# Kernel optimization log

Measured on AMD Instinct MI355X. Metric: run time of the kernel, lower is better.

## Reference

```python
import jax, jax.numpy as jnp
import numpy as np

TAU = [1, 2, 4, 8]
B, T, FC, FX = 128, 2048, 512, 512


def setup_inputs() -> dict:
    key = jax.random.key(0)
    k1, k2, k3, k4 = jax.random.split(key, 4)
    C = jax.random.normal(k1, (B, T, FC), dtype=jnp.float32)
    X = jax.random.normal(k2, (B, T, FX), dtype=jnp.float32)
    # one Linear(encoding_size -> context_size) per tau; torch weight layout [out, in]
    W = jax.random.normal(k3, (len(TAU), FC, FX), dtype=jnp.float32) * (1.0 / np.sqrt(FX))
    b = jax.random.normal(k4, (len(TAU), FC), dtype=jnp.float32) * 0.01
    return {"C": C, "X": X, "W": W, "b": b}


def _infonce(Ct, Xe, Wk, bk):
    # Ct: [B, Tt, fc], Xe: [B, Tt, fx]
    Xt = jnp.einsum('btf,gf->btg', Xe, Wk) + bk          # Linear: [B, Tt, fc]
    Z = jnp.einsum('itf,jtf->ijt', Ct, Xt)               # scores [B, B, Tt]
    Zmax = jnp.max(Z, axis=1, keepdims=True)             # [B, 1, Tt]
    lse = jnp.log(jnp.sum(jnp.exp(Z - Zmax), axis=1)) + Zmax[:, 0]  # [B, Tt]
    Zdiag = jnp.diagonal(Z, axis1=0, axis2=1).T          # Z[i,i,t] -> [B, Tt]
    return jnp.mean(Zdiag - lse)


def reference(C, X, W, b):
    losses = [_infonce(C[:, :-t], X[:, t:], W[k], b[k]) for k, t in enumerate(TAU)]
    return jnp.stack(losses)
```

## Files before the change

### kernel.cpp

```cpp
#include <hip/hip_runtime.h>
#include <math.h>

constexpr int Tn  = 2048;
constexpr int FCn = 512;
constexpr int FXn = 512;
constexpr int SXW = 72;
constexpr int SYC = 136;
constexpr int SZS = 132;

typedef __attribute__((ext_vector_type(8))) short  bf16x8;
typedef __attribute__((ext_vector_type(4))) float  f32x4;

__device__ __forceinline__ unsigned pk2(float a, float b) {
  return __builtin_amdgcn_perm(__float_as_uint(b), __float_as_uint(a), 0x07060302u);
}
__device__ __forceinline__ uint4 pack8(float4 a, float4 b) {
  uint4 rv;
  rv.x = pk2(a.x, a.y); rv.y = pk2(a.z, a.w);
  rv.z = pk2(b.x, b.y); rv.w = pk2(b.z, b.w);
  return rv;
}

__device__ __forceinline__ void gll16(const unsigned short* g, void* lds) {
  __builtin_amdgcn_global_load_lds(
      (const __attribute__((address_space(1))) unsigned int*)g,
      (__attribute__((address_space(3))) unsigned int*)lds, 16, 0, 0);
}

__global__ void zero4(float* out) {
  if (threadIdx.x < 4) out[threadIdx.x] = 0.0f;
}

__global__ void finalize4(float* out) {
  int k = threadIdx.x;
  if (k < 4) out[k] *= 1.0f / (128.0f * (float)(Tn - (1 << k)));
}

__global__ void tobf16(const float* __restrict__ s, unsigned short* __restrict__ d) {
  int i = blockIdx.x * 256 + threadIdx.x;
  float4 v = ((const float4*)s)[i];
  uint2 p; p.x = pk2(v.x, v.y); p.y = pk2(v.z, v.w);
  ((uint2*)d)[i] = p;
}

__global__ __launch_bounds__(256, 2)
void infonce_v7(const float* __restrict__ Cp, const unsigned short* __restrict__ Xb,
                const unsigned short* __restrict__ Wb, float* __restrict__ out)
{
  __shared__ __align__(16) unsigned char smem[67648];
  char* sm   = (char*)smem;
  char* sWc  = sm + 16384;
  float* sZ  = (float*)sm;
  float* sRed = (float*)(sm + 67584);

  const int tid  = threadIdx.x;
  const int lane = tid & 63;
  const int wave = tid >> 6;
  const int r    = lane & 15;
  const int h    = lane >> 4;
  const int jw   = wave >> 1;
  const int gw   = wave & 1;
  const int iw   = wave >> 1;
  const int jw2  = wave & 1;

  const int orig = blockIdx.x;
  const int xcd  = orig & 7;
  const int loc  = orig >> 3;
  const int wg   = (xcd < 4) ? (xcd * 1024 + loc) : (4096 + (xcd - 4) * 1023 + loc);
  const int k    = wg & 3;
  const int t    = wg >> 2;
  const int tau  = 1 << k;
  if (t >= Tn - tau) return;
  const int s = t + tau;

  const int colg = (lane & 7) ^ (lane >> 3);
  const unsigned short* xlane = Xb + (size_t)(wave * 32 + (lane >> 3)) * (Tn * FXn)
                                + (size_t)s * FXn + colg * 8;
  const unsigned short* wlane = Wb + (size_t)k * (FCn * FXn)
                                + (size_t)(wave * 64 + (lane >> 3)) * FXn + colg * 8;
  char* xdst = sm  + wave * 4096;
  char* wdst = sWc + wave * 8192;

  const float* cr0 = Cp + (size_t)(iw * 64 +  0 + r) * (Tn * FCn) + (size_t)t * FCn;
  const float* cr1 = Cp + (size_t)(iw * 64 + 16 + r) * (Tn * FCn) + (size_t)t * FCn;
  const float* cr2 = Cp + (size_t)(iw * 64 + 32 + r) * (Tn * FCn) + (size_t)t * FCn;
  const float* cr3 = Cp + (size_t)(iw * 64 + 48 + r) * (Tn * FCn) + (size_t)t * FCn;

  f32x4 zacc[4][4];
#pragma unroll
  for (int a = 0; a < 4; ++a)
#pragma unroll
    for (int b = 0; b < 4; ++b) zacc[a][b] = f32x4{0.f, 0.f, 0.f, 0.f};

#pragma unroll 1
  for (int gc = 0; gc < 2; ++gc) {
    f32x4 yacc[4][8];
#pragma unroll
    for (int a = 0; a < 4; ++a)
#pragma unroll
      for (int b = 0; b < 8; ++b) yacc[a][b] = f32x4{0.f, 0.f, 0.f, 0.f};

#pragma unroll 1
    for (int xc = 0; xc < 8; ++xc) {
      __syncthreads();
#pragma unroll
      for (int i = 0; i < 4; ++i)
        gll16(xlane + (size_t)(i * 8) * (Tn * FXn) + xc * 64, xdst + i * 1024);
#pragma unroll
      for (int i = 0; i < 8; ++i)
        gll16(wlane + (size_t)(gc * 256 + i * 8) * FXn + xc * 64, wdst + i * 1024);
      __syncthreads();
#pragma unroll
      for (int ks = 0; ks < 2; ++ks) {
        const int cbx = (ks * 64 + h * 16) ^ ((r & 7) << 4);
        bf16x8 ax[4], bw[8];
#pragma unroll
        for (int bm = 0; bm < 4; ++bm)
          ax[bm] = *(const bf16x8*)(sm + (jw * 64 + bm * 16 + r) * 128 + cbx);
#pragma unroll
        for (int bn = 0; bn < 8; ++bn)
          bw[bn] = *(const bf16x8*)(sWc + (gw * 128 + bn * 16 + r) * 128 + cbx);
#pragma unroll
        for (int bm = 0; bm < 4; ++bm)
#pragma unroll
          for (int bn = 0; bn < 8; ++bn)
            yacc[bm][bn] = __builtin_amdgcn_mfma_f32_16x16x32_bf16(
                ax[bm], bw[bn], yacc[bm][bn], 0, 0, 0);
      }
    }
    __syncthreads();
#pragma unroll
    for (int bm = 0; bm < 4; ++bm)
#pragma unroll
      for (int bn = 0; bn < 8; ++bn)
#pragma unroll
        for (int reg = 0; reg < 4; ++reg) {
          const int row = jw * 64 + bm * 16 + h * 4 + reg;
          const int col = gw * 128 + bn * 16 + r;
          *(unsigned short*)(sm + row * 528 + col * 2) =
              (unsigned short)(__float_as_uint(yacc[bm][bn][reg]) >> 16);
        }
    __syncthreads();
#pragma unroll 2
    for (int ks2 = 0; ks2 < 8; ++ks2) {
      const int goff = gc * 256 + ks2 * 32 + h * 8;
      const int gb   = ks2 * 64 + h * 16;
      bf16x8 ac[4], by[4];
      {
        float4 u0 = *(const float4*)(cr0 + goff);
        float4 v0 = *(const float4*)(cr0 + goff + 4);
        float4 u1 = *(const float4*)(cr1 + goff);
        float4 v1 = *(const float4*)(cr1 + goff + 4);
        float4 u2 = *(const float4*)(cr2 + goff);
        float4 v2 = *(const float4*)(cr2 + goff + 4);
        float4 u3 = *(const float4*)(cr3 + goff);
        float4 v3 = *(const float4*)(cr3 + goff + 4);
        ac[0] = __builtin_bit_cast(bf16x8, pack8(u0, v0));
        ac[1] = __builtin_bit_cast(bf16x8, pack8(u1, v1));
        ac[2] = __builtin_bit_cast(bf16x8, pack8(u2, v2));
        ac[3] = __builtin_bit_cast(bf16x8, pack8(u3, v3));
      }
#pragma unroll
      for (int bn = 0; bn < 4; ++bn)
        by[bn] = *(const bf16x8*)(sm + (jw2 * 64 + bn * 16 + r) * 528 + gb);
#pragma unroll
      for (int bm = 0; bm < 4; ++bm)
#pragma unroll
        for (int bn = 0; bn < 4; ++bn)
          zacc[bm][bn] = __builtin_amdgcn_mfma_f32_16x16x32_bf16(
              ac[bm], by[bn], zacc[bm][bn], 0, 0, 0);
    }
  }
  __syncthreads();
#pragma unroll
  for (int bm = 0; bm < 4; ++bm)
#pragma unroll
    for (int bn = 0; bn < 4; ++bn)
#pragma unroll
      for (int reg = 0; reg < 4; ++reg)
        sZ[(iw * 64 + bm * 16 + h * 4 + reg) * SZS + (jw2 * 64 + bn * 16 + r)] =
            zacc[bm][bn][reg];
  __syncthreads();

  const int row = wave * 32 + (lane >> 1);
  const int c0l = lane & 1;
  float mx = -3.4e38f;
#pragma unroll
  for (int m = 0; m < 64; ++m) mx = fmaxf(mx, sZ[row * SZS + c0l + m * 2]);
  mx = fmaxf(mx, __shfl_xor(mx, 1));
  float sum = 0.f;
#pragma unroll
  for (int m = 0; m < 64; ++m) sum += __expf(sZ[row * SZS + c0l + m * 2] - mx);
  sum += __shfl_xor(sum, 1);
  float val = (c0l == 0) ? (sZ[row * SZS + row] - (__logf(sum) + mx)) : 0.f;
#pragma unroll
  for (int off = 1; off < 64; off <<= 1) val += __shfl_xor(val, off);
  if (lane == 0) sRed[wave] = val;
  __syncthreads();
  if (tid == 0) atomicAdd(out + k, sRed[0] + sRed[1] + sRed[2] + sRed[3]);
}

template <bool WBF>
__global__ __launch_bounds__(512, 4)
void infonce_main(const float* __restrict__ Cp, const float* __restrict__ Xp,
                  const void* __restrict__ Wp, float* __restrict__ out)
{
  __shared__ __align__(16) unsigned char smem[71680];
  unsigned short* sX = (unsigned short*)(smem);
  unsigned short* sW = (unsigned short*)(smem + 18432);
  unsigned short* sY = (unsigned short*)(smem + 36864);
  unsigned short* sC = (unsigned short*)(smem);
  float* sZ   = (float*)(smem);
  float* sRed = (float*)(smem + 67584);

  const int tid  = threadIdx.x;
  const int lane = tid & 63;
  const int wave = tid >> 6;
  const int r    = lane & 15;
  const int h    = lane >> 4;
  const int wr   = wave >> 1;
  const int wc   = wave & 1;

  const int orig = blockIdx.x;
  const int xcd  = orig & 7;
  const int loc  = orig >> 3;
  const int wg   = (xcd < 4) ? (xcd * 1024 + loc) : (4096 + (xcd - 4) * 1023 + loc);
  const int k    = wg & 3;
  const int t    = wg >> 2;
  const int tau  = 1 << k;
  if (t >= Tn - tau) return;

  const float* Cb = Cp + (size_t)t * FCn;
  const float* Xb = Xp + (size_t)(t + tau) * FXn;

  const int srow = tid >> 2;
  const int scol = (tid & 3) * 16;
  const float* xs = Xb + (size_t)srow * (Tn * FXn) + scol;
  unsigned short* xd = sX + srow * SXW + scol;
  unsigned short* wd = sW + srow * SXW + scol;
  const unsigned short* wsh = (const unsigned short*)Wp + (size_t)k * (FCn * FXn)
                              + (size_t)srow * FXn + scol;
  const float* wsf = (const float*)Wp + (size_t)k * (FCn * FXn)
                     + (size_t)srow * FXn + scol;
  const int crow0 = tid >> 4;
  const int ccol  = (tid & 15) * 8;
  const float* cs = Cb + (size_t)crow0 * (Tn * FCn) + ccol;
  unsigned short* cd = sC + crow0 * SYC + ccol;
  const size_t cstep = (size_t)32 * Tn * FCn;

  float4 px0, px1, px2, px3;
  float4 pw0, pw1, pw2, pw3;
  uint4  pb0, pb1;
  float4 pc0, pc1, pc2, pc3, pc4, pc5, pc6, pc7;

#define LOAD_X(XC) do { \
    const float4* _p = (const float4*)(xs + (XC) * 64); \
    px0 = _p[0]; px1 = _p[1]; px2 = _p[2]; px3 = _p[3]; } while (0)
#define LOAD_W(GC, XC) do { \
    if constexpr (WBF) { \
      const uint4* _p = (const uint4*)(wsh + (size_t)((GC) * 128) * FXn + (XC) * 64); \
      pb0 = _p[0]; pb1 = _p[1]; \
    } else { \
      const float4* _p = (const float4*)(wsf + (size_t)((GC) * 128) * FXn + (XC) * 64); \
      pw0 = _p[0]; pw1 = _p[1]; pw2 = _p[2]; pw3 = _p[3]; } } while (0)
#define STORE_XW() do { \
    *(uint4*)(xd)     = pack8(px0, px1); \
    *(uint4*)(xd + 8) = pack8(px2, px3); \
    if constexpr (WBF) { *(uint4*)(wd) = pb0; *(uint4*)(wd + 8) = pb1; } \
    else { *(uint4*)(wd) = pack8(pw0, pw1); *(uint4*)(wd + 8) = pack8(pw2, pw3); } \
  } while (0)
#define MFMA_Y() do { \
    _Pragma("unroll") \
    for (int ks = 0; ks < 2; ++ks) { \
      const int xoo = ks * 32 + h * 8; \
      bf16x8 a0 = *(const bf16x8*)(sX + (wr * 32 + 0  + r) * SXW + xoo); \
      bf16x8 a1 = *(const bf16x8*)(sX + (wr * 32 + 16 + r) * SXW + xoo); \
      _Pragma("unroll") \
      for (int bg = 0; bg < 4; ++bg) { \
        bf16x8 bb = *(const bf16x8*)(sW + (wc * 64 + bg * 16 + r) * SXW + xoo); \
        yacc[0][bg] = __builtin_amdgcn_mfma_f32_16x16x32_bf16(a0, bb, yacc[0][bg], 0, 0, 0); \
        yacc[1][bg] = __builtin_amdgcn_mfma_f32_16x16x32_bf16(a1, bb, yacc[1][bg], 0, 0, 0); \
      } } } while (0)

  f32x4 zacc[2][4];
#pragma unroll
  for (int a = 0; a < 2; ++a)
#pragma unroll
    for (int b = 0; b < 4; ++b) zacc[a][b] = f32x4{0.f, 0.f, 0.f, 0.f};

  LOAD_X(0); LOAD_W(0, 0);

  for (int gc = 0; gc < 4; ++gc) {
    f32x4 yacc[2][4];
#pragma unroll
    for (int a = 0; a < 2; ++a)
#pragma unroll
      for (int b = 0; b < 4; ++b) yacc[a][b] = f32x4{0.f, 0.f, 0.f, 0.f};

    for (int xc = 0; xc < 7; ++xc) {
      __syncthreads();
      STORE_XW();
      __syncthreads();
      LOAD_X(xc + 1); LOAD_W(gc, xc + 1);
      MFMA_Y();
    }
    __syncthreads();
    STORE_XW();
    __syncthreads();
    {
      const float4* p0 = (const float4*)(cs + 0 * cstep + gc * 128);
      const float4* p1 = (const float4*)(cs + 1 * cstep + gc * 128);
      const float4* p2 = (const float4*)(cs + 2 * cstep + gc * 128);
      const float4* p3 = (const float4*)(cs + 3 * cstep + gc * 128);
      pc0 = p0[0]; pc1 = p0[1];
      pc2 = p1[0]; pc3 = p1[1];
      pc4 = p2[0]; pc5 = p2[1];
      pc6 = p3[0]; pc7 = p3[1];
    }
    MFMA_Y();

#pragma unroll
    for (int aj = 0; aj < 2; ++aj)
#pragma unroll
      for (int bg = 0; bg < 4; ++bg)
#pragma unroll
        for (int reg = 0; reg < 4; ++reg)
          sY[(wr * 32 + aj * 16 + h * 4 + reg) * SYC + (wc * 64 + bg * 16 + r)] =
              (unsigned short)(__float_as_uint(yacc[aj][bg][reg]) >> 16);
    __syncthreads();
    *(uint4*)(cd + 0 * 32 * SYC) = pack8(pc0, pc1);
    *(uint4*)(cd + 1 * 32 * SYC) = pack8(pc2, pc3);
    *(uint4*)(cd + 2 * 32 * SYC) = pack8(pc4, pc5);
    *(uint4*)(cd + 3 * 32 * SYC) = pack8(pc6, pc7);
    __syncthreads();
    if (gc < 3) { LOAD_X(0); LOAD_W(gc + 1, 0); }
#pragma unroll
    for (int ks = 0; ks < 4; ++ks) {
      const int go = ks * 32 + h * 8;
      bf16x8 a0 = *(const bf16x8*)(sC + (wr * 32 + 0  + r) * SYC + go);
      bf16x8 a1 = *(const bf16x8*)(sC + (wr * 32 + 16 + r) * SYC + go);
#pragma unroll
      for (int bj = 0; bj < 4; ++bj) {
        bf16x8 bb = *(const bf16x8*)(sY + (wc * 64 + bj * 16 + r) * SYC + go);
        zacc[0][bj] = __builtin_amdgcn_mfma_f32_16x16x32_bf16(a0, bb, zacc[0][bj], 0, 0, 0);
        zacc[1][bj] = __builtin_amdgcn_mfma_f32_16x16x32_bf16(a1, bb, zacc[1][bj], 0, 0, 0);
      }
    }
  }
  __syncthreads();
#pragma unroll
  for (int ai = 0; ai < 2; ++ai)
#pragma unroll
    for (int bj = 0; bj < 4; ++bj)
#pragma unroll
      for (int reg = 0; reg < 4; ++reg)
        sZ[(wr * 32 + ai * 16 + h * 4 + reg) * SZS + (wc * 64 + bj * 16 + r)] =
            zacc[ai][bj][reg];
  __syncthreads();

  const int row = wave * 16 + (lane >> 2);
  const int c0l = lane & 3;
  float mx = -3.4e38f;
#pragma unroll
  for (int m = 0; m < 32; ++m) mx = fmaxf(mx, sZ[row * SZS + c0l + m * 4]);
  mx = fmaxf(mx, __shfl_xor(mx, 1));
  mx = fmaxf(mx, __shfl_xor(mx, 2));
  float sum = 0.f;
#pragma unroll
  for (int m = 0; m < 32; ++m) sum += __expf(sZ[row * SZS + c0l + m * 4] - mx);
  sum += __shfl_xor(sum, 1);
  sum += __shfl_xor(sum, 2);
  float val = (c0l == 0) ? (sZ[row * SZS + row] - (__logf(sum) + mx)) : 0.f;
#pragma unroll
  for (int off = 1; off < 64; off <<= 1) val += __shfl_xor(val, off);
  if (lane == 0) sRed[wave] = val;
  __syncthreads();
  if (tid == 0) {
    float bs = 0.f;
#pragma unroll
    for (int w2 = 0; w2 < 8; ++w2) bs += sRed[w2];
    atomicAdd(out + k, bs);
  }
#undef LOAD_X
#undef LOAD_W
#undef STORE_XW
#undef MFMA_Y
}

extern "C" void kernel_launch(void* const* d_in, const int* in_sizes, int n_in,
                              void* d_out, int out_size, void* d_ws, size_t ws_size,
                              hipStream_t stream) {
  const float* C = (const float*)d_in[0];
  const float* X = (const float*)d_in[1];
  const float* W = (const float*)d_in[2];
  float* out = (float*)d_out;

  const size_t NX = (size_t)128 * Tn * FXn;
  const size_t NW = (size_t)4 * FCn * FXn;
  const size_t WS_W   = NW * 2;
  const size_t WS_MID = WS_W + NX * 2;

  hipLaunchKernelGGL(zero4, dim3(1), dim3(64), 0, stream, out);

  if (ws_size >= WS_MID) {
    unsigned short* Wbf = (unsigned short*)d_ws;
    unsigned short* Xbf = (unsigned short*)((char*)d_ws + WS_W);
    hipLaunchKernelGGL(tobf16, dim3((unsigned)(NW / 1024)), dim3(256), 0, stream, W, Wbf);
    hipLaunchKernelGGL(tobf16, dim3((unsigned)(NX / 1024)), dim3(256), 0, stream, X, Xbf);
    hipLaunchKernelGGL(infonce_v7, dim3(2047 * 4), dim3(256), 0, stream,
                       C, Xbf, Wbf, out);
  } else if (ws_size >= WS_W) {
    hipLaunchKernelGGL(tobf16, dim3((unsigned)(NW / 1024)), dim3(256), 0, stream,
                       W, (unsigned short*)d_ws);
    hipLaunchKernelGGL(infonce_main<true>, dim3(2047 * 4), dim3(512), 0, stream,
                       C, X, (const void*)d_ws, out);
  } else {
    hipLaunchKernelGGL(infonce_main<false>, dim3(2047 * 4), dim3(512), 0, stream,
                       C, X, (const void*)W, out);
  }
  hipLaunchKernelGGL(finalize4, dim3(1), dim3(64), 0, stream, out);
}
```

Measured before the change: 1.364 ms.

## Double-buffer X/W staging and compute softmax stats from MFMA registers

The projection GEMM now stages X and W in 32-element k-chunks into two LDS buffers. The next chunk's global_load_lds is issued before the current chunk's MFMAs, so load latency overlaps compute and each step needs one barrier instead of two. The Y tile is stored in LDS with an XOR swizzle instead of padded rows. The final logsumexp now reduces max and sum directly from the Z accumulator registers using lane shuffles and a small cross-wave stats exchange, which avoids the full Z round trip through LDS. The cost is more LDS buffer bookkeeping and extra shuffle and barrier steps in the epilogue.

```diff
diff --git a/kernel.cpp b/kernel.cpp
--- a/kernel.cpp
+++ b/kernel.cpp
@@ -44,24 +44,24 @@
 }
 
 __global__ __launch_bounds__(256, 2)
-void infonce_v7(const float* __restrict__ Cp, const unsigned short* __restrict__ Xb,
+void infonce_v8(const float* __restrict__ Cp, const unsigned short* __restrict__ Xb,
                 const unsigned short* __restrict__ Wb, float* __restrict__ out)
 {
   __shared__ __align__(16) unsigned char smem[67648];
-  char* sm   = (char*)smem;
-  char* sWc  = sm + 16384;
-  float* sZ  = (float*)sm;
-  float* sRed = (float*)(sm + 67584);
-
-  const int tid  = threadIdx.x;
-  const int lane = tid & 63;
-  const int wave = tid >> 6;
-  const int r    = lane & 15;
-  const int h    = lane >> 4;
-  const int jw   = wave >> 1;
-  const int gw   = wave & 1;
-  const int iw   = wave >> 1;
-  const int jw2  = wave & 1;
+  char* sm = (char*)smem;
+  float* stats_m = (float*)(sm + 65536);
+  float* stats_s = (float*)(sm + 66560);
+  float* sRed    = (float*)(sm + 67584);
+
+  const int tid = threadIdx.x;
+  const int l   = tid & 63;
+  const int w   = tid >> 6;
+  const int r   = l & 15;
+  const int h   = l >> 4;
+  const int jw  = w >> 1;
+  const int gw  = w & 1;
+  const int iw  = w >> 1;
+  const int jw2 = w & 1;
 
   const int orig = blockIdx.x;
   const int xcd  = orig & 7;
@@ -73,62 +73,83 @@
   if (t >= Tn - tau) return;
   const int s = t + tau;
 
-  const int colg = (lane & 7) ^ (lane >> 3);
-  const unsigned short* xlane = Xb + (size_t)(wave * 32 + (lane >> 3)) * (Tn * FXn)
-                                + (size_t)s * FXn + colg * 8;
-  const unsigned short* wlane = Wb + (size_t)k * (FCn * FXn)
-                                + (size_t)(wave * 64 + (lane >> 3)) * FXn + colg * 8;
-  char* xdst = sm  + wave * 4096;
-  char* wdst = sWc + wave * 8192;
-
-  const float* cr0 = Cp + (size_t)(iw * 64 +  0 + r) * (Tn * FCn) + (size_t)t * FCn;
-  const float* cr1 = Cp + (size_t)(iw * 64 + 16 + r) * (Tn * FCn) + (size_t)t * FCn;
-  const float* cr2 = Cp + (size_t)(iw * 64 + 32 + r) * (Tn * FCn) + (size_t)t * FCn;
-  const float* cr3 = Cp + (size_t)(iw * 64 + 48 + r) * (Tn * FCn) + (size_t)t * FCn;
+  const int sub = l >> 2;
+  const int gsw = (l & 3) ^ ((l >> 3) & 3);
+  const size_t xstr = (size_t)Tn * FXn;
+  const unsigned short* xs0 = Xb + (size_t)(w * 32 + sub) * xstr
+                              + (size_t)s * FXn + gsw * 8;
+  const unsigned short* xs1 = xs0 + (size_t)16 * xstr;
+  const unsigned short* wk  = Wb + (size_t)k * (FCn * FXn) + gsw * 8;
+  const unsigned short* ws0 = wk  + (size_t)(w * 64 + sub) * FXn;
+  const unsigned short* ws1 = ws0 + (size_t)16 * FXn;
+  const unsigned short* ws2 = ws0 + (size_t)32 * FXn;
+  const unsigned short* ws3 = ws0 + (size_t)48 * FXn;
+
+  const size_t cstr = (size_t)Tn * FCn;
+  const float* cr0 = Cp + (size_t)(iw * 64 +  0 + r) * cstr + (size_t)t * FCn;
+  const float* cr1 = Cp + (size_t)(iw * 64 + 16 + r) * cstr + (size_t)t * FCn;
+  const float* cr2 = Cp + (size_t)(iw * 64 + 32 + r) * cstr + (size_t)t * FCn;
+  const float* cr3 = Cp + (size_t)(iw * 64 + 48 + r) * cstr + (size_t)t * FCn;
 
   f32x4 zacc[4][4];
 #pragma unroll
   for (int a = 0; a < 4; ++a)
 #pragma unroll
     for (int b = 0; b < 4; ++b) zacc[a][b] = f32x4{0.f, 0.f, 0.f, 0.f};
+
+#define STG8(BUFC, XC) do { \
+    char* _bb = sm + (BUFC) * 24576; \
+    const size_t _xo = (size_t)(XC) * 32; \
+    gll16(xs0 + _xo, _bb + (w * 2    ) * 1024); \
+    gll16(xs1 + _xo, _bb + (w * 2 + 1) * 1024); \
+    const size_t _wo = wgc + _xo; \
+    gll16(ws0 + _wo, _bb + 8192 + (w * 4    ) * 1024); \
+    gll16(ws1 + _wo, _bb + 8192 + (w * 4 + 1) * 1024); \
+    gll16(ws2 + _wo, _bb + 8192 + (w * 4 + 2) * 1024); \
+    gll16(ws3 + _wo, _bb + 8192 + (w * 4 + 3) * 1024); \
+  } while (0)
+
+#define MFY8(BUFC) do { \
+    const char* _bx = sm + (BUFC) * 24576; \
+    const char* _bw = _bx + 8192; \
+    const int _gb = (h ^ ((r >> 1) & 3)) << 4; \
+    bf16x8 _ax[4]; \
+    _Pragma("unroll") \
+    for (int _bm = 0; _bm < 4; ++_bm) \
+      _ax[_bm] = *(const bf16x8*)(_bx + (jw * 64 + _bm * 16 + r) * 64 + _gb); \
+    bf16x8 _bv[8]; \
+    _Pragma("unroll") \
+    for (int _bn = 0; _bn < 8; ++_bn) \
+      _bv[_bn] = *(const bf16x8*)(_bw + (gw * 128 + _bn * 16 + r) * 64 + _gb); \
+    _Pragma("unroll") \
+    for (int _bm = 0; _bm < 4; ++_bm) \
+      _Pragma("unroll") \
+      for (int _bn = 0; _bn < 8; ++_bn) \
+        yacc[_bm][_bn] = __builtin_amdgcn_mfma_f32_16x16x32_bf16( \
+            _ax[_bm], _bv[_bn], yacc[_bm][_bn], 0, 0, 0); \
+  } while (0)
 
 #pragma unroll 1
   for (int gc = 0; gc < 2; ++gc) {
+    const size_t wgc = (size_t)gc * 256 * FXn;
     f32x4 yacc[4][8];
 #pragma unroll
     for (int a = 0; a < 4; ++a)
 #pragma unroll
       for (int b = 0; b < 8; ++b) yacc[a][b] = f32x4{0.f, 0.f, 0.f, 0.f};
 
+    STG8(0, 0);
+    __syncthreads();
 #pragma unroll 1
-    for (int xc = 0; xc < 8; ++xc) {
+    for (int xc2 = 0; xc2 < 8; ++xc2) {
+      STG8(1, 2 * xc2 + 1);
+      MFY8(0);
       __syncthreads();
-#pragma unroll
-      for (int i = 0; i < 4; ++i)
-        gll16(xlane + (size_t)(i * 8) * (Tn * FXn) + xc * 64, xdst + i * 1024);
-#pragma unroll
-      for (int i = 0; i < 8; ++i)
-        gll16(wlane + (size_t)(gc * 256 + i * 8) * FXn + xc * 64, wdst + i * 1024);
+      if (xc2 < 7) STG8(0, 2 * xc2 + 2);
+      MFY8(1);
       __syncthreads();
-#pragma unroll
-      for (int ks = 0; ks < 2; ++ks) {
-        const int cbx = (ks * 64 + h * 16) ^ ((r & 7) << 4);
-        bf16x8 ax[4], bw[8];
-#pragma unroll
-        for (int bm = 0; bm < 4; ++bm)
-          ax[bm] = *(const bf16x8*)(sm + (jw * 64 + bm * 16 + r) * 128 + cbx);
-#pragma unroll
-        for (int bn = 0; bn < 8; ++bn)
-          bw[bn] = *(const bf16x8*)(sWc + (gw * 128 + bn * 16 + r) * 128 + cbx);
-#pragma unroll
-        for (int bm = 0; bm < 4; ++bm)
-#pragma unroll
-          for (int bn = 0; bn < 8; ++bn)
-            yacc[bm][bn] = __builtin_amdgcn_mfma_f32_16x16x32_bf16(
-                ax[bm], bw[bn], yacc[bm][bn], 0, 0, 0);
-      }
-    }
-    __syncthreads();
+    }
+
 #pragma unroll
     for (int bm = 0; bm < 4; ++bm)
 #pragma unroll
@@ -137,67 +158,98 @@
         for (int reg = 0; reg < 4; ++reg) {
           const int row = jw * 64 + bm * 16 + h * 4 + reg;
           const int col = gw * 128 + bn * 16 + r;
-          *(unsigned short*)(sm + row * 528 + col * 2) =
+          *(unsigned short*)(sm + row * 512 + ((col * 2) ^ ((row & 7) << 4))) =
               (unsigned short)(__float_as_uint(yacc[bm][bn][reg]) >> 16);
         }
     __syncthreads();
+
+    const int swz = (r & 7) << 4;
 #pragma unroll 2
     for (int ks2 = 0; ks2 < 8; ++ks2) {
       const int goff = gc * 256 + ks2 * 32 + h * 8;
-      const int gb   = ks2 * 64 + h * 16;
-      bf16x8 ac[4], by[4];
-      {
-        float4 u0 = *(const float4*)(cr0 + goff);
-        float4 v0 = *(const float4*)(cr0 + goff + 4);
-        float4 u1 = *(const float4*)(cr1 + goff);
-        float4 v1 = *(const float4*)(cr1 + goff + 4);
-        float4 u2 = *(const float4*)(cr2 + goff);
-        float4 v2 = *(const float4*)(cr2 + goff + 4);
-        float4 u3 = *(const float4*)(cr3 + goff);
-        float4 v3 = *(const float4*)(cr3 + goff + 4);
-        ac[0] = __builtin_bit_cast(bf16x8, pack8(u0, v0));
-        ac[1] = __builtin_bit_cast(bf16x8, pack8(u1, v1));
-        ac[2] = __builtin_bit_cast(bf16x8, pack8(u2, v2));
-        ac[3] = __builtin_bit_cast(bf16x8, pack8(u3, v3));
-      }
+      float4 u0 = *(const float4*)(cr0 + goff), p0 = *(const float4*)(cr0 + goff + 4);
+      float4 u1 = *(const float4*)(cr1 + goff), p1 = *(const float4*)(cr1 + goff + 4);
+      float4 u2 = *(const float4*)(cr2 + goff), p2 = *(const float4*)(cr2 + goff + 4);
+      float4 u3 = *(const float4*)(cr3 + goff), p3 = *(const float4*)(cr3 + goff + 4);
+      bf16x8 acv[4];
+      acv[0] = __builtin_bit_cast(bf16x8, pack8(u0, p0));
+      acv[1] = __builtin_bit_cast(bf16x8, pack8(u1, p1));
+      acv[2] = __builtin_bit_cast(bf16x8, pack8(u2, p2));
+      acv[3] = __builtin_bit_cast(bf16x8, pack8(u3, p3));
+      const int gb = ks2 * 64 + h * 16;
+      bf16x8 byv[4];
 #pragma unroll
       for (int bn = 0; bn < 4; ++bn)
-        by[bn] = *(const bf16x8*)(sm + (jw2 * 64 + bn * 16 + r) * 528 + gb);
+        byv[bn] = *(const bf16x8*)(sm + (jw2 * 64 + bn * 16 + r) * 512 + (gb ^ swz));
 #pragma unroll
       for (int bm = 0; bm < 4; ++bm)
 #pragma unroll
         for (int bn = 0; bn < 4; ++bn)
           zacc[bm][bn] = __builtin_amdgcn_mfma_f32_16x16x32_bf16(
-              ac[bm], by[bn], zacc[bm][bn], 0, 0, 0);
-    }
+              acv[bm], byv[bn], zacc[bm][bn], 0, 0, 0);
+    }
+    __syncthreads();
   }
-  __syncthreads();
+
+  float gm[4][4], tot[4][4];
 #pragma unroll
   for (int bm = 0; bm < 4; ++bm)
 #pragma unroll
-    for (int bn = 0; bn < 4; ++bn)
+    for (int reg = 0; reg < 4; ++reg) {
+      float m = fmaxf(fmaxf(zacc[bm][0][reg], zacc[bm][1][reg]),
+                      fmaxf(zacc[bm][2][reg], zacc[bm][3][reg]));
+      m = fmaxf(m, __shfl_xor(m, 1));
+      m = fmaxf(m, __shfl_xor(m, 2));
+      m = fmaxf(m, __shfl_xor(m, 4));
+      m = fmaxf(m, __shfl_xor(m, 8));
+      gm[bm][reg] = m;
+      if (r == 0) stats_m[jw2 * 128 + iw * 64 + bm * 16 + h * 4 + reg] = m;
+    }
+  __syncthreads();
+#pragma unroll
+  for (int bm = 0; bm < 4; ++bm)
+#pragma unroll
+    for (int reg = 0; reg < 4; ++reg)
+      gm[bm][reg] = fmaxf(gm[bm][reg],
+          stats_m[(jw2 ^ 1) * 128 + iw * 64 + bm * 16 + h * 4 + reg]);
+#pragma unroll
+  for (int bm = 0; bm < 4; ++bm)
+#pragma unroll
+    for (int reg = 0; reg < 4; ++reg) {
+      float sv = __expf(zacc[bm][0][reg] - gm[bm][reg])
+               + __expf(zacc[bm][1][reg] - gm[bm][reg])
+               + __expf(zacc[bm][2][reg] - gm[bm][reg])
+               + __expf(zacc[bm][3][reg] - gm[bm][reg]);
+      sv += __shfl_xor(sv, 1);
+      sv += __shfl_xor(sv, 2);
+      sv += __shfl_xor(sv, 4);
+      sv += __shfl_xor(sv, 8);
+      tot[bm][reg] = sv;
+      if (r == 0) stats_s[jw2 * 128 + iw * 64 + bm * 16 + h * 4 + reg] = sv;
+    }
+  __syncthreads();
+#pragma unroll
+  for (int bm = 0; bm < 4; ++bm)
+#pragma unroll
+    for (int reg = 0; reg < 4; ++reg)
+      tot[bm][reg] += stats_s[(jw2 ^ 1) * 128 + iw * 64 + bm * 16 + h * 4 + reg];
+
+  float val = 0.f;
+  if (iw == jw2) {
+#pragma unroll
+    for (int bm = 0; bm < 4; ++bm)
 #pragma unroll
       for (int reg = 0; reg < 4; ++reg)
-        sZ[(iw * 64 + bm * 16 + h * 4 + reg) * SZS + (jw2 * 64 + bn * 16 + r)] =
-            zacc[bm][bn][reg];
-  __syncthreads();
-
-  const int row = wave * 32 + (lane >> 1);
-  const int c0l = lane & 1;
-  float mx = -3.4e38f;
-#pragma unroll
-  for (int m = 0; m < 64; ++m) mx = fmaxf(mx, sZ[row * SZS + c0l + m * 2]);
-  mx = fmaxf(mx, __shfl_xor(mx, 1));
-  float sum = 0.f;
-#pragma unroll
-  for (int m = 0; m < 64; ++m) sum += __expf(sZ[row * SZS + c0l + m * 2] - mx);
-  sum += __shfl_xor(sum, 1);
-  float val = (c0l == 0) ? (sZ[row * SZS + row] - (__logf(sum) + mx)) : 0.f;
+        if (r == h * 4 + reg)
+          val += zacc[bm][bm][reg] - (__logf(tot[bm][reg]) + gm[bm][reg]);
+  }
 #pragma unroll
   for (int off = 1; off < 64; off <<= 1) val += __shfl_xor(val, off);
-  if (lane == 0) sRed[wave] = val;
+  if (l == 0) sRed[w] = val;
   __syncthreads();
   if (tid == 0) atomicAdd(out + k, sRed[0] + sRed[1] + sRed[2] + sRed[3]);
+#undef STG8
+#undef MFY8
 }
 
 template <bool WBF>
@@ -269,7 +321,7 @@
     if constexpr (WBF) { *(uint4*)(wd) = pb0; *(uint4*)(wd + 8) = pb1; } \
     else { *(uint4*)(wd) = pack8(pw0, pw1); *(uint4*)(wd + 8) = pack8(pw2, pw3); } \
   } while (0)
-#define MFMA_Y() do { \
+#define MFMA_YF() do { \
     _Pragma("unroll") \
     for (int ks = 0; ks < 2; ++ks) { \
       const int xoo = ks * 32 + h * 8; \
@@ -302,7 +354,7 @@
       STORE_XW();
       __syncthreads();
       LOAD_X(xc + 1); LOAD_W(gc, xc + 1);
-      MFMA_Y();
+      MFMA_YF();
     }
     __syncthreads();
     STORE_XW();
@@ -317,7 +369,7 @@
       pc4 = p2[0]; pc5 = p2[1];
       pc6 = p3[0]; pc7 = p3[1];
     }
-    MFMA_Y();
+    MFMA_YF();
 
 #pragma unroll
     for (int aj = 0; aj < 2; ++aj)
@@ -384,7 +436,7 @@
 #undef LOAD_X
 #undef LOAD_W
 #undef STORE_XW
-#undef MFMA_Y
+#undef MFMA_YF
 }
 
 extern "C" void kernel_launch(void* const* d_in, const int* in_sizes, int n_in,
@@ -407,7 +459,7 @@
     unsigned short* Xbf = (unsigned short*)((char*)d_ws + WS_W);
     hipLaunchKernelGGL(tobf16, dim3((unsigned)(NW / 1024)), dim3(256), 0, stream, W, Wbf);
     hipLaunchKernelGGL(tobf16, dim3((unsigned)(NX / 1024)), dim3(256), 0, stream, X, Xbf);
-    hipLaunchKernelGGL(infonce_v7, dim3(2047 * 4), dim3(256), 0, stream,
+    hipLaunchKernelGGL(infonce_v8, dim3(2047 * 4), dim3(256), 0, stream,
                        C, Xbf, Wbf, out);
   } else if (ws_size >= WS_W) {
     hipLaunchKernelGGL(tobf16, dim3((unsigned)(NW / 1024)), dim3(256), 0, stream,
```

Measured after the change: 2.153 ms. +57.9%, slower.
